# Optimization experiments

Hardware: AMD Instinct MI355X
Metric: run time of the kernel (lower is better)

## Reference

```python
import jax, jax.numpy as jnp
import numpy as np

IN_DIM = 256
LN_EPS = 1e-05


def _xavier(key, shape):
    fan_in, fan_out = shape[1], shape[0]
    a = np.sqrt(6.0 / (fan_in + fan_out)).astype(np.float32)
    return jax.random.uniform(key, shape, jnp.float32, -a, a)


def setup_inputs() -> dict:
    key = jax.random.key(0)
    ks = jax.random.split(key, 4)
    B, C, H, W = 32, IN_DIM, 32, 32
    x = jax.random.normal(ks[0], (B, C, H, W), jnp.float32)
    y = jax.random.normal(ks[1], (B, C, H, W), jnp.float32)
    # nn.MultiheadAttention in_proj: rows [0:C] -> Wq, [C:2C] -> Wk (V/out_proj
    # never influence the returned attention weights, so omitted).
    Wq = _xavier(ks[2], (C, C))
    Wk = _xavier(ks[3], (C, C))
    bq = jnp.zeros((C,), jnp.float32)
    bk = jnp.zeros((C,), jnp.float32)
    # norm1 LayerNorm affine params (norm2 is unused in forward).
    gamma = jnp.ones((C,), jnp.float32)
    beta = jnp.zeros((C,), jnp.float32)
    return {"x": x, "y": y, "gamma": gamma, "beta": beta,
            "Wq": Wq, "Wk": Wk, "bq": bq, "bk": bk}


def _layernorm(t, gamma, beta):
    mu = jnp.mean(t, axis=-1, keepdims=True)
    var = jnp.mean(jnp.square(t - mu), axis=-1, keepdims=True)
    return (t - mu) * jax.lax.rsqrt(var + LN_EPS) * gamma + beta


def reference(x, y, gamma, beta, Wq, Wk, bq, bk):
    B, C = x.shape[0], x.shape[1]
    # [B,C,H,W] -> [B, N, C]
    xs = x.reshape(B, C, -1).transpose(0, 2, 1)
    ys = y.reshape(B, C, -1).transpose(0, 2, 1)
    q = _layernorm(xs, gamma, beta) @ Wq.T + bq   # [B,N,C]
    k = _layernorm(ys, gamma, beta) @ Wk.T + bk   # [B,N,C]
    scale = 1.0 / np.sqrt(C).astype(np.float32)   # single head: head_dim = C
    scores = jnp.einsum('bnc,bmc->bnm', q, k) * scale  # [B,N,N]
    w = jax.nn.softmax(scores, axis=-1)
    # module returns weight.diagonal(dim1=1, dim2=2) -> [B, N]
    return jnp.diagonal(w, axis1=1, axis2=2)
```

## Files before the change

### kernel.cpp

```cpp
#include <hip/hip_runtime.h>
#include <math.h>

#define BATCH 32
#define CDIM  256
#define NDIM  1024
#define BN    (BATCH * NDIM)
#define BNC   ((size_t)BATCH * NDIM * CDIM)
#define LN_EPSF 1e-5f
#define SCALE 0.0625f

typedef __attribute__((ext_vector_type(8))) __bf16 bf16x8;
typedef __attribute__((ext_vector_type(4))) float f32x4;
typedef __attribute__((ext_vector_type(4))) unsigned short ushort4v;

static __device__ __forceinline__ unsigned short f2bf(float f) {
  unsigned u = __float_as_uint(f);
  unsigned r = (u + 0x7FFFu + ((u >> 16) & 1u)) >> 16;
  return (unsigned short)r;
}
static __device__ __forceinline__ float bf2f(unsigned short h) {
  return __uint_as_float(((unsigned)h) << 16);
}
static __device__ __forceinline__ void gload16(const void* g, void* l) {
  __builtin_amdgcn_global_load_lds((const __attribute__((address_space(1))) void*)g,
                                   (__attribute__((address_space(3))) void*)l, 16, 0, 0);
}


__global__ __launch_bounds__(256) void wsplit_k(const float* __restrict__ Wq,
                                                const float* __restrict__ Wk,
                                                unsigned short* __restrict__ wp) {
  int idx = blockIdx.x * 256 + threadIdx.x;
  float vq = Wq[idx];
  unsigned short hq = f2bf(vq);
  wp[idx] = hq;
  wp[65536 + idx] = f2bf(vq - bf2f(hq));
  float vk = Wk[idx];
  unsigned short hk = f2bf(vk);
  wp[131072 + idx] = hk;
  wp[196608 + idx] = f2bf(vk - bf2f(hk));
}

__global__ __launch_bounds__(256) void proj_k(const float* __restrict__ x,
                                              const float* __restrict__ y,
                                              const float* __restrict__ gamma,
                                              const float* __restrict__ beta,
                                              const float* __restrict__ bq,
                                              const float* __restrict__ bk,
                                              const unsigned short* __restrict__ wp,
                                              unsigned short* __restrict__ planes) {
  __shared__ unsigned short Lh[64][264];
  __shared__ unsigned short Ll[64][264];
  __shared__ float psum[16][64], psq[16][64];
  __shared__ float mu[64], ri[64], gl[CDIM], bl[CDIM], bias_s[CDIM];

  const int t = threadIdx.x;
  const int bz = blockIdx.y;
  const int b = bz >> 1, which = bz & 1;
  const int n0 = blockIdx.x * 64;
  const float* src = which ? y : x;

  gl[t] = gamma[t];
  bl[t] = beta[t];
  bias_s[t] = (which ? bk : bq)[t];

  const int nq = (t & 15) * 4;
  const int cs = (t >> 4) * 16;
  float4 xr[16];
#pragma unroll
  for (int i = 0; i < 16; ++i)
    xr[i] = *(const float4*)(src + ((size_t)b * CDIM + cs + i) * NDIM + n0 + nq);

  {
    float s[4] = {0.f, 0.f, 0.f, 0.f}, q[4] = {0.f, 0.f, 0.f, 0.f};
#pragma unroll
    for (int i = 0; i < 16; ++i) {
      float v0 = xr[i].x, v1 = xr[i].y, v2 = xr[i].z, v3 = xr[i].w;
      s[0] += v0; q[0] += v0 * v0;
      s[1] += v1; q[1] += v1 * v1;
      s[2] += v2; q[2] += v2 * v2;
      s[3] += v3; q[3] += v3 * v3;
    }
#pragma unroll
    for (int j = 0; j < 4; ++j) {
      psum[t >> 4][nq + j] = s[j];
      psq[t >> 4][nq + j] = q[j];
    }
  }
  __syncthreads();
  if (t < 64) {
    float S = 0.f, Q = 0.f;
#pragma unroll
    for (int s16 = 0; s16 < 16; ++s16) { S += psum[s16][t]; Q += psq[s16][t]; }
    float m = S * (1.f / CDIM);
    mu[t] = m;
    ri[t] = rsqrtf(fmaxf(Q * (1.f / CDIM) - m * m, 0.f) + LN_EPSF);
  }
  __syncthreads();

  {
    float mj[4], rj[4];
#pragma unroll
    for (int j = 0; j < 4; ++j) { mj[j] = mu[nq + j]; rj[j] = ri[nq + j]; }
#pragma unroll
    for (int k = 0; k < 8; ++k) {
      const int c0 = cs + 2 * k, c1 = c0 + 1;
      const float g0 = gl[c0], b0 = bl[c0], g1 = gl[c1], b1 = bl[c1];
      const float u0[4] = {xr[2 * k].x, xr[2 * k].y, xr[2 * k].z, xr[2 * k].w};
      const float u1[4] = {xr[2 * k + 1].x, xr[2 * k + 1].y, xr[2 * k + 1].z, xr[2 * k + 1].w};
#pragma unroll
      for (int j = 0; j < 4; ++j) {
        float v0 = (u0[j] - mj[j]) * rj[j] * g0 + b0;
        float v1 = (u1[j] - mj[j]) * rj[j] * g1 + b1;
        unsigned short h0 = f2bf(v0), h1 = f2bf(v1);
        unsigned short e0 = f2bf(v0 - bf2f(h0)), e1 = f2bf(v1 - bf2f(h1));
        *(unsigned*)&Lh[nq + j][c0] = ((unsigned)h1 << 16) | h0;
        *(unsigned*)&Ll[nq + j][c0] = ((unsigned)e1 << 16) | e0;
      }
    }
  }
  __syncthreads();

  const int w = t >> 6, l = t & 63;
  const int l15 = l & 15, l4 = l >> 4;
  const int co_base = w * 64;
  const unsigned short* Wh = wp + (size_t)which * 131072;
  const unsigned short* Wl = Wh + 65536;

  f32x4 acc[4][4];
#pragma unroll
  for (int i = 0; i < 4; ++i)
#pragma unroll
    for (int j = 0; j < 4; ++j) acc[i][j] = (f32x4){0.f, 0.f, 0.f, 0.f};

#pragma unroll
  for (int kt = 0; kt < 8; ++kt) {
    const int c0 = kt * 32;
    bf16x8 Ah[4], Al[4], Bh[4], Bl[4];
#pragma unroll
    for (int i = 0; i < 4; ++i) {
      size_t off = (size_t)(co_base + i * 16 + l15) * CDIM + c0 + l4 * 8;
      Ah[i] = *(const bf16x8*)(Wh + off);
      Al[i] = *(const bf16x8*)(Wl + off);
    }
#pragma unroll
    for (int j = 0; j < 4; ++j) {
      Bh[j] = *(const bf16x8*)&Lh[j * 16 + l15][c0 + l4 * 8];
      Bl[j] = *(const bf16x8*)&Ll[j * 16 + l15][c0 + l4 * 8];
    }
#pragma unroll
    for (int i = 0; i < 4; ++i)
#pragma unroll
      for (int j = 0; j < 4; ++j) {
        acc[i][j] = __builtin_amdgcn_mfma_f32_16x16x32_bf16(Ah[i], Bh[j], acc[i][j], 0, 0, 0);
        acc[i][j] = __builtin_amdgcn_mfma_f32_16x16x32_bf16(Ah[i], Bl[j], acc[i][j], 0, 0, 0);
        acc[i][j] = __builtin_amdgcn_mfma_f32_16x16x32_bf16(Al[i], Bh[j], acc[i][j], 0, 0, 0);
      }
  }

  unsigned short* ph = planes + (size_t)which * (2 * BNC);
  unsigned short* pl = ph + BNC;
#pragma unroll
  for (int i = 0; i < 4; ++i) {
    const int co4 = co_base + i * 16 + l4 * 4;
    float bias4[4];
#pragma unroll
    for (int r = 0; r < 4; ++r) bias4[r] = bias_s[co4 + r];
#pragma unroll
    for (int j = 0; j < 4; ++j) {
      size_t base = ((size_t)b * NDIM + n0 + j * 16 + l15) * CDIM + co4;
      ushort4v hs, ls;
#pragma unroll
      for (int r = 0; r < 4; ++r) {
        float v = acc[i][j][r] + bias4[r];
        unsigned short h = f2bf(v);
        hs[r] = h;
        ls[r] = f2bf(v - bf2f(h));
      }
      *(ushort4v*)(ph + base) = hs;
      *(ushort4v*)(pl + base) = ls;
    }
  }
}

__global__ __launch_bounds__(256) void attn_k(const unsigned short* __restrict__ planes,
                                              float* __restrict__ outp) {
  const unsigned short* qh = planes;
  const unsigned short* ql = planes + BNC;
  const unsigned short* kh = planes + 2 * BNC;
  const unsigned short* kl = planes + 3 * BNC;
  __shared__ unsigned short kbuf[2][2][4096];

  const int p = blockIdx.x;
  const int b = (p & 7) * 4 + ((p >> 3) & 3);
  const int n0 = (p >> 5) * 64;
  const int t = threadIdx.x;
  const int wid = t >> 6;
  const int l = t & 63;
  const int l15 = l & 15, l4 = l >> 4;

  bf16x8 ah[8], al[8];
  {
    size_t rowbase = ((size_t)b * NDIM + n0 + wid * 16 + l15) * CDIM + l4 * 8;
#pragma unroll
    for (int kt = 0; kt < 8; ++kt) {
      ah[kt] = *(const bf16x8*)(qh + rowbase + kt * 32);
      al[kt] = *(const bf16x8*)(ql + rowbase + kt * 32);
    }
  }

  auto stage = [&](int buf, int mt, int kt) {
#pragma unroll
    for (int ii = 0; ii < 2; ++ii) {
      const int fr = wid * 2 + ii;
      size_t g = ((size_t)b * NDIM + mt * 128 + fr * 16 + l15) * CDIM + kt * 32 + l4 * 8;
      gload16(kh + g, &kbuf[buf][0][fr * 512]);
      gload16(kl + g, &kbuf[buf][1][fr * 512]);
    }
  };

  float M[4], S[4], dval[4];
#pragma unroll
  for (int r = 0; r < 4; ++r) { M[r] = -1e30f; S[r] = 0.f; dval[r] = 0.f; }

  stage(0, 0, 0);
  __syncthreads();
  int cur = 0;

  for (int mt = 0; mt < 8; ++mt) {
    f32x4 acc[8];
#pragma unroll
    for (int f = 0; f < 8; ++f) acc[f] = (f32x4){0.f, 0.f, 0.f, 0.f};

    for (int kt = 0; kt < 8; ++kt) {
      const int tt = mt * 8 + kt;
      if (tt + 1 < 64) stage(cur ^ 1, (tt + 1) >> 3, (tt + 1) & 7);
      const unsigned short* bhp = &kbuf[cur][0][0];
      const unsigned short* blp = &kbuf[cur][1][0];
#pragma unroll
      for (int f = 0; f < 8; ++f) {
        bf16x8 Bh = *(const bf16x8*)(bhp + f * 512 + l * 8);
        bf16x8 Bl = *(const bf16x8*)(blp + f * 512 + l * 8);
        acc[f] = __builtin_amdgcn_mfma_f32_16x16x32_bf16(ah[kt], Bh, acc[f], 0, 0, 0);
        acc[f] = __builtin_amdgcn_mfma_f32_16x16x32_bf16(ah[kt], Bl, acc[f], 0, 0, 0);
        acc[f] = __builtin_amdgcn_mfma_f32_16x16x32_bf16(al[kt], Bh, acc[f], 0, 0, 0);
      }
      __syncthreads();
      cur ^= 1;
    }

    const int nrow = n0 + wid * 16 + l4 * 4;
#pragma unroll
    for (int r = 0; r < 4; ++r) {
      const int n = nrow + r;
      float tm = -1e30f;
#pragma unroll
      for (int f = 0; f < 8; ++f) tm = fmaxf(tm, acc[f][r]);
      tm *= SCALE;
#pragma unroll
      for (int off = 8; off >= 1; off >>= 1) tm = fmaxf(tm, __shfl_xor(tm, off));
      const float Mn = fmaxf(M[r], tm);
      float ps = 0.f;
#pragma unroll
      for (int f = 0; f < 8; ++f) ps += __expf(acc[f][r] * SCALE - Mn);
#pragma unroll
      for (int off = 8; off >= 1; off >>= 1) ps += __shfl_xor(ps, off);
      S[r] = S[r] * __expf(M[r] - Mn) + ps;
      M[r] = Mn;
#pragma unroll
      for (int f = 0; f < 8; ++f)
        if (mt * 128 + f * 16 + l15 == n) dval[r] = acc[f][r] * SCALE;
    }
  }

#pragma unroll
  for (int r = 0; r < 4; ++r) {
    const int n = n0 + wid * 16 + l4 * 4 + r;
    if ((n & 15) == l15)
      outp[(size_t)b * NDIM + n] = __expf(dval[r] - M[r]) / S[r];
  }
}

extern "C" void kernel_launch(void* const* d_in, const int* in_sizes, int n_in,
                              void* d_out, int out_size, void* d_ws, size_t ws_size,
                              hipStream_t stream) {
  (void)in_sizes; (void)n_in; (void)out_size; (void)ws_size;
  const float* x     = (const float*)d_in[0];
  const float* y     = (const float*)d_in[1];
  const float* gamma = (const float*)d_in[2];
  const float* beta  = (const float*)d_in[3];
  const float* Wq    = (const float*)d_in[4];
  const float* Wk    = (const float*)d_in[5];
  const float* bq    = (const float*)d_in[6];
  const float* bk    = (const float*)d_in[7];
  float* out = (float*)d_out;

  unsigned short* wp = (unsigned short*)d_ws;
  unsigned short* planes = wp + 262144;

  wsplit_k<<<256, 256, 0, stream>>>(Wq, Wk, wp);

  dim3 g2(NDIM / 64, BATCH * 2);
  proj_k<<<g2, 256, 0, stream>>>(x, y, gamma, beta, bq, bk, wp, planes);

  attn_k<<<512, 256, 0, stream>>>(planes, out);
}
```

Before: 222.1 us.

## Load K fragments directly from global into registers, dropping LDS staging

The attention kernel no longer stages K-high/K-low tiles into shared memory through global_load_lds with double buffering and per-step barriers. Each wave now loads its B fragments straight from global memory into registers, using two register sets to prefetch the next k-step while computing the current one. This removes the LDS round trip and the __syncthreads calls. The cost is that all four waves of a block load the same K data separately, which multiplies global/L2 traffic by four and raises register pressure.

```diff
diff --git a/kernel.cpp b/kernel.cpp
--- a/kernel.cpp
+++ b/kernel.cpp
@@ -20,10 +20,6 @@
 }
 static __device__ __forceinline__ float bf2f(unsigned short h) {
   return __uint_as_float(((unsigned)h) << 16);
-}
-static __device__ __forceinline__ void gload16(const void* g, void* l) {
-  __builtin_amdgcn_global_load_lds((const __attribute__((address_space(1))) void*)g,
-                                   (__attribute__((address_space(3))) void*)l, 16, 0, 0);
 }
 
 
@@ -187,9 +183,6 @@
                                               float* __restrict__ outp) {
   const unsigned short* qh = planes;
   const unsigned short* ql = planes + BNC;
-  const unsigned short* kh = planes + 2 * BNC;
-  const unsigned short* kl = planes + 3 * BNC;
-  __shared__ unsigned short kbuf[2][2][4096];
 
   const int p = blockIdx.x;
   const int b = (p & 7) * 4 + ((p >> 3) & 3);
@@ -209,44 +202,44 @@
     }
   }
 
-  auto stage = [&](int buf, int mt, int kt) {
-#pragma unroll
-    for (int ii = 0; ii < 2; ++ii) {
-      const int fr = wid * 2 + ii;
-      size_t g = ((size_t)b * NDIM + mt * 128 + fr * 16 + l15) * CDIM + kt * 32 + l4 * 8;
-      gload16(kh + g, &kbuf[buf][0][fr * 512]);
-      gload16(kl + g, &kbuf[buf][1][fr * 512]);
-    }
-  };
+  const unsigned short* kb = planes + 2 * BNC + (size_t)b * NDIM * CDIM;
+  const unsigned short* lb = planes + 3 * BNC + (size_t)b * NDIM * CDIM;
 
   float M[4], S[4], dval[4];
 #pragma unroll
   for (int r = 0; r < 4; ++r) { M[r] = -1e30f; S[r] = 0.f; dval[r] = 0.f; }
-
-  stage(0, 0, 0);
-  __syncthreads();
-  int cur = 0;
 
   for (int mt = 0; mt < 8; ++mt) {
     f32x4 acc[8];
 #pragma unroll
     for (int f = 0; f < 8; ++f) acc[f] = (f32x4){0.f, 0.f, 0.f, 0.f};
 
-    for (int kt = 0; kt < 8; ++kt) {
-      const int tt = mt * 8 + kt;
-      if (tt + 1 < 64) stage(cur ^ 1, (tt + 1) >> 3, (tt + 1) & 7);
-      const unsigned short* bhp = &kbuf[cur][0][0];
-      const unsigned short* blp = &kbuf[cur][1][0];
+    auto loadk = [&](int kt, bf16x8 (&BH)[8], bf16x8 (&BL)[8]) {
 #pragma unroll
       for (int f = 0; f < 8; ++f) {
-        bf16x8 Bh = *(const bf16x8*)(bhp + f * 512 + l * 8);
-        bf16x8 Bl = *(const bf16x8*)(blp + f * 512 + l * 8);
-        acc[f] = __builtin_amdgcn_mfma_f32_16x16x32_bf16(ah[kt], Bh, acc[f], 0, 0, 0);
-        acc[f] = __builtin_amdgcn_mfma_f32_16x16x32_bf16(ah[kt], Bl, acc[f], 0, 0, 0);
-        acc[f] = __builtin_amdgcn_mfma_f32_16x16x32_bf16(al[kt], Bh, acc[f], 0, 0, 0);
-      }
-      __syncthreads();
-      cur ^= 1;
+        size_t off = (size_t)(mt * 128 + f * 16 + l15) * CDIM + kt * 32 + l4 * 8;
+        BH[f] = *(const bf16x8*)(kb + off);
+        BL[f] = *(const bf16x8*)(lb + off);
+      }
+    };
+    auto step = [&](int kt, bf16x8 (&BH)[8], bf16x8 (&BL)[8]) {
+#pragma unroll
+      for (int f = 0; f < 8; ++f) {
+        acc[f] = __builtin_amdgcn_mfma_f32_16x16x32_bf16(ah[kt], BH[f], acc[f], 0, 0, 0);
+        acc[f] = __builtin_amdgcn_mfma_f32_16x16x32_bf16(ah[kt], BL[f], acc[f], 0, 0, 0);
+        acc[f] = __builtin_amdgcn_mfma_f32_16x16x32_bf16(al[kt], BH[f], acc[f], 0, 0, 0);
+      }
+    };
+
+    bf16x8 BA[8], LA[8], BB[8], LB[8];
+    loadk(0, BA, LA);
+    loadk(1, BB, LB);
+#pragma unroll
+    for (int kk = 0; kk < 8; kk += 2) {
+      step(kk, BA, LA);
+      if (kk + 2 < 8) loadk(kk + 2, BA, LA);
+      step(kk + 1, BB, LB);
+      if (kk + 3 < 8) loadk(kk + 3, BB, LB);
     }
 
     const int nrow = n0 + wid * 16 + l4 * 4;
```

Result: slower. 383.0 us (+72.4%).
